# Performance work log

Hardware: AMD Instinct MI355X
Metric: run time of the kernel (lower is better)

The kernel has to match this reference:

```python
import jax, jax.numpy as jnp
import numpy as np

N = 100000   # nodes (in_ch)
D = 128      # emb_ch
E = 1600000  # nonzeros in A_hat
RATE = 0.1   # dropout rate


def setup_inputs() -> dict:
    key = jax.random.key(0)
    k1, k2, k3, k4, k5, k6 = jax.random.split(key, 6)
    x = jnp.arange(N, dtype=jnp.int64) if jax.config.jax_enable_x64 else jnp.arange(N, dtype=jnp.int32)
    rows = jax.random.randint(k1, (E,), 0, N)
    cols = jax.random.randint(k2, (E,), 0, N)
    A_vals = jax.random.uniform(k3, (E,), dtype=jnp.float32)
    # xavier_uniform for [N, D]: bound = sqrt(6/(N+D))
    bound = float(np.sqrt(6.0 / (N + D)))
    emb_weight = jax.random.uniform(k4, (N, D), jnp.float32, -bound, bound)
    u1 = jax.random.uniform(k5, (N, D), dtype=jnp.float32)
    u2 = jax.random.uniform(k6, (N, D), dtype=jnp.float32)
    return {"x": x, "rows": rows, "cols": cols, "A_vals": A_vals,
            "emb_weight": emb_weight, "u1": u1, "u2": u2}


def _dropout(h, u):
    keep = (u >= RATE).astype(h.dtype)
    return h * keep / (1.0 - RATE)


def _spmm(rows, cols, vals, h):
    # out[i] = sum_{e: rows[e]==i} vals[e] * h[cols[e]]  -- COO SpMM
    msgs = vals[:, None] * h[cols]  # [E, D]
    return jax.ops.segment_sum(msgs, rows, num_segments=N)


def reference(x, rows, cols, A_vals, emb_weight, u1, u2):
    h0 = emb_weight[x]                       # embedding lookup [N, D]
    h1 = _spmm(rows, cols, A_vals, _dropout(h0, u1))
    h2 = _spmm(rows, cols, A_vals, _dropout(h1, u2))
    return (h0 + h1 + h2) / 3.0
```

## Files before the change

### kernel.cpp

```cpp
#include <hip/hip_runtime.h>
#include <hip/hip_fp16.h>

#define DD 128
#define SCAN_CHUNK 1024
#define G_ROWS 32
#define G_STAGE 1024

typedef float          f32x4 __attribute__((ext_vector_type(4)));
typedef unsigned int   u32x4 __attribute__((ext_vector_type(4)));
typedef unsigned int   u32x2 __attribute__((ext_vector_type(2)));
typedef unsigned short u16x8 __attribute__((ext_vector_type(8)));

struct __align__(8) Edge { int c; float v; };

__device__ __forceinline__ unsigned short f2h(float f) {
    return __half_as_ushort(__float2half(f));
}
__device__ __forceinline__ float2 up2(unsigned int u) {
    __half2 h = *reinterpret_cast<const __half2*>(&u);
    return __half22float2(h);
}

template <typename T>
__device__ __forceinline__ T ldnt(const T* p) { return __builtin_nontemporal_load(p); }
template <typename T>
__device__ __forceinline__ void stnt(T* p, T v) { __builtin_nontemporal_store(v, p); }

__global__ __launch_bounds__(256) void k_g1hist(const float* __restrict__ emb,
                                                const float* __restrict__ u1,
                                                ushort* __restrict__ g1,
                                                const int* __restrict__ rows,
                                                unsigned int* __restrict__ cnt16,
                                                ushort* __restrict__ rank,
                                                int total8, int E) {
    int i = blockIdx.x * 256 + threadIdx.x;
    bool doE = i < E;
    bool doS = i < total8;
    int r = 0;
    if (doE) r = ldnt(rows + i);
    f32x4 hA, hB, uA, uB;
    if (doS) {
        const f32x4* e4 = (const f32x4*)emb;
        const f32x4* a4 = (const f32x4*)u1;
        hA = ldnt(e4 + 2 * (size_t)i);
        hB = ldnt(e4 + 2 * (size_t)i + 1);
        uA = ldnt(a4 + 2 * (size_t)i);
        uB = ldnt(a4 + 2 * (size_t)i + 1);
    }
    if (doE) {
        int sh = (r & 1) << 4;
        unsigned int old = atomicAdd(&cnt16[r >> 1], 1u << sh);
        stnt(rank + i, (ushort)((old >> sh) & 0xFFFFu));
    }
    if (doS) {
        const float s = 1.0f / 0.9f;
        u16x8 g;
        g[0] = f2h((uA.x >= 0.1f) ? hA.x * s : 0.0f);
        g[1] = f2h((uA.y >= 0.1f) ? hA.y * s : 0.0f);
        g[2] = f2h((uA.z >= 0.1f) ? hA.z * s : 0.0f);
        g[3] = f2h((uA.w >= 0.1f) ? hA.w * s : 0.0f);
        g[4] = f2h((uB.x >= 0.1f) ? hB.x * s : 0.0f);
        g[5] = f2h((uB.y >= 0.1f) ? hB.y * s : 0.0f);
        g[6] = f2h((uB.z >= 0.1f) ? hB.z * s : 0.0f);
        g[7] = f2h((uB.w >= 0.1f) ? hB.w * s : 0.0f);
        ((u16x8*)g1)[i] = g;
    }
}

__global__ __launch_bounds__(256) void k_scan1(const unsigned int* __restrict__ cnt16,
                                               int* __restrict__ rs,
                                               int* __restrict__ bsum, int n) {
    __shared__ int s[256];
    int tid = threadIdx.x;
    int base = blockIdx.x * SCAN_CHUNK + tid * 4;
    int c0 = 0, c1 = 0, c2 = 0, c3 = 0;
    if (base < n) {
        unsigned int w0 = cnt16[base >> 1];
        c0 = (int)(w0 & 0xFFFFu);
        c1 = (int)(w0 >> 16);
    }
    if (base + 2 < n) {
        unsigned int w1 = cnt16[(base >> 1) + 1];
        c2 = (int)(w1 & 0xFFFFu);
        c3 = (int)(w1 >> 16);
    }
    int tsum = c0 + c1 + c2 + c3;
    s[tid] = tsum;
    __syncthreads();
    for (int off = 1; off < 256; off <<= 1) {
        int t = (tid >= off) ? s[tid - off] : 0;
        __syncthreads();
        s[tid] += t;
        __syncthreads();
    }
    int excl = s[tid] - tsum;
    if (tid == 255) bsum[blockIdx.x] = s[255];
    if (base < n)     rs[base]     = excl;
    if (base + 1 < n) rs[base + 1] = excl + c0;
    if (base + 2 < n) rs[base + 2] = excl + c0 + c1;
    if (base + 3 < n) rs[base + 3] = excl + c0 + c1 + c2;
}

__global__ __launch_bounds__(256) void k_scan23(int* __restrict__ rs,
                                                const int* __restrict__ bsum,
                                                int nb, int n) {
    __shared__ int s[1024];
    int tid = threadIdx.x;
    for (int i = tid; i < nb; i += 256) s[i] = bsum[i];
    __syncthreads();
    if (tid == 0) {
        int run = 0;
        for (int i = 0; i < nb; ++i) { int t = s[i]; s[i] = run; run += t; }
    }
    __syncthreads();
    int i = blockIdx.x * 256 + tid;
    if (i < n) rs[i] += s[i >> 10];
}

__global__ __launch_bounds__(256) void k_scatter_prep(const int* __restrict__ rows,
                                                      const int* __restrict__ cols,
                                                      const float* __restrict__ vals,
                                                      const int* __restrict__ rs,
                                                      const ushort* __restrict__ rank,
                                                      Edge* __restrict__ ev,
                                                      const float* __restrict__ emb,
                                                      const float* __restrict__ u2,
                                                      ushort* __restrict__ emb16,
                                                      unsigned char* __restrict__ mask2,
                                                      int E, int total8) {
    int i = blockIdx.x * 256 + threadIdx.x;
    bool doE = i < E;
    bool doS = i < total8;
    int r = 0, c = 0; float vv = 0.f; unsigned int rk = 0;
    if (doE) {
        r = ldnt(rows + i);
        c = ldnt(cols + i);
        vv = ldnt(vals + i);
        rk = ldnt(rank + i);
    }
    f32x4 hA, hB, vA, vB;
    if (doS) {
        const f32x4* e4 = (const f32x4*)emb;
        const f32x4* b4 = (const f32x4*)u2;
        hA = ldnt(e4 + 2 * (size_t)i);
        hB = ldnt(e4 + 2 * (size_t)i + 1);
        vA = ldnt(b4 + 2 * (size_t)i);
        vB = ldnt(b4 + 2 * (size_t)i + 1);
    }
    if (doE) {
        int pos = rs[r] + (int)rk;
        u32x2 q;
        q.x = (unsigned int)c;
        q.y = __float_as_uint(vv);
        ((u32x2*)ev)[pos] = q;
    }
    if (doS) {
        u16x8 e16;
        e16[0] = f2h(hA.x); e16[1] = f2h(hA.y); e16[2] = f2h(hA.z); e16[3] = f2h(hA.w);
        e16[4] = f2h(hB.x); e16[5] = f2h(hB.y); e16[6] = f2h(hB.z); e16[7] = f2h(hB.w);
        stnt((u16x8*)emb16 + i, e16);
        unsigned char m =
            (unsigned char)((vA.x >= 0.1f ? 1u : 0u)  | (vA.y >= 0.1f ? 2u : 0u)  |
                            (vA.z >= 0.1f ? 4u : 0u)  | (vA.w >= 0.1f ? 8u : 0u)  |
                            (vB.x >= 0.1f ? 16u : 0u) | (vB.y >= 0.1f ? 32u : 0u) |
                            (vB.z >= 0.1f ? 64u : 0u) | (vB.w >= 0.1f ? 128u : 0u));
        stnt(mask2 + i, m);
    }
}

template <int MODE>
__global__ __launch_bounds__(256) void k_gather(const int* __restrict__ rowstart,
                                                const Edge* __restrict__ ev,
                                                const ushort* __restrict__ srch,
                                                const unsigned char* __restrict__ mask2,
                                                const ushort* __restrict__ emb16,
                                                const ushort* __restrict__ p16in,
                                                ushort* __restrict__ p16out,
                                                ushort* __restrict__ g2,
                                                float* __restrict__ out,
                                                int N, int E) {
    __shared__ int s_rs[G_ROWS + 1];
    __shared__ Edge s_ev[G_STAGE];

    int tid = threadIdx.x;
    int r0 = blockIdx.x * G_ROWS;
    int h = blockIdx.y;
    if (tid <= G_ROWS) {
        int r = r0 + tid;
        s_rs[tid] = (r < N) ? rowstart[r] : E;
    }
    __syncthreads();
    int base = s_rs[0];
    int nblk = s_rs[G_ROWS] - base;
    int nstage = nblk < G_STAGE ? nblk : G_STAGE;
    for (int i = tid; i < nstage; i += 256) {
        u32x2 q = ldnt((const u32x2*)(ev + base + i));
        Edge ed; ed.c = (int)q.x; ed.v = __uint_as_float(q.y);
        s_ev[i] = ed;
    }
    __syncthreads();

    int grp = tid >> 3;
    int lane = tid & 7;
    int row = r0 + grp;
    if (row >= N) return;
    int start = s_rs[grp] - base;
    int end = s_rs[grp + 1] - base;
    int eL = end < nstage ? end : nstage;

    const u32x4* __restrict__ s4 = (const u32x4*)srch;
    const Edge* __restrict__ evg = ev + base;
    int hoff = (h << 3) + lane;
    float a0 = 0.f, a1 = 0.f, a2 = 0.f, a3 = 0.f;
    float a4 = 0.f, a5 = 0.f, a6 = 0.f, a7 = 0.f;

#define LDE(i) Edge E##i = s_ev[e + i]; float fv##i = E##i.v;
#define LDP(i) int ix##i = e + i; bool ok##i = ix##i < eL; \
               Edge E##i = s_ev[ok##i ? ix##i : last]; \
               float fv##i = ok##i ? E##i.v : 0.0f;
#define GQ(i)  u32x4 q##i = s4[((size_t)E##i.c << 4) + hoff];
#define ACC(i) { float vv = fv##i; \
        float2 w0 = up2(q##i.x), w1 = up2(q##i.y), w2 = up2(q##i.z), w3 = up2(q##i.w); \
        a0 = fmaf(vv, w0.x, a0); a1 = fmaf(vv, w0.y, a1); \
        a2 = fmaf(vv, w1.x, a2); a3 = fmaf(vv, w1.y, a3); \
        a4 = fmaf(vv, w2.x, a4); a5 = fmaf(vv, w2.y, a5); \
        a6 = fmaf(vv, w3.x, a6); a7 = fmaf(vv, w3.y, a7); }

    int e = start;
    for (; e + 8 <= eL; e += 8) {
        LDE(0) LDE(1) LDE(2) LDE(3) LDE(4) LDE(5) LDE(6) LDE(7)
        GQ(0) GQ(1) GQ(2) GQ(3) GQ(4) GQ(5) GQ(6) GQ(7)
        ACC(0) ACC(1) ACC(2) ACC(3) ACC(4) ACC(5) ACC(6) ACC(7)
    }
    if (e < eL) {
        int last = eL - 1;
        LDP(0) LDP(1) LDP(2) LDP(3) LDP(4) LDP(5) LDP(6) LDP(7)
        GQ(0) GQ(1) GQ(2) GQ(3) GQ(4) GQ(5) GQ(6) GQ(7)
        ACC(0) ACC(1) ACC(2) ACC(3) ACC(4) ACC(5) ACC(6) ACC(7)
        e = eL;
    }
    for (; e < end; ++e) {
        Edge E0; { u32x2 q_ = ldnt((const u32x2*)(evg + e));
                   E0.c = (int)q_.x; E0.v = __uint_as_float(q_.y); }
        float fv0 = E0.v;
        GQ(0) ACC(0)
    }
#undef LDE
#undef LDP
#undef GQ
#undef ACC

    size_t o = ((size_t)row << 7) + ((size_t)h << 6) + (size_t)lane * 8;
    if (MODE == 1) {
        unsigned int m = mask2[(size_t)row * 16 + (h << 3) + lane];
        const float s = 1.0f / 0.9f;
        u16x8 gg;
        gg[0] = (m & 1u)   ? f2h(a0 * s) : (ushort)0;
        gg[1] = (m & 2u)   ? f2h(a1 * s) : (ushort)0;
        gg[2] = (m & 4u)   ? f2h(a2 * s) : (ushort)0;
        gg[3] = (m & 8u)   ? f2h(a3 * s) : (ushort)0;
        gg[4] = (m & 16u)  ? f2h(a4 * s) : (ushort)0;
        gg[5] = (m & 32u)  ? f2h(a5 * s) : (ushort)0;
        gg[6] = (m & 64u)  ? f2h(a6 * s) : (ushort)0;
        gg[7] = (m & 128u) ? f2h(a7 * s) : (ushort)0;
        stnt((u16x8*)(g2 + o), gg);
        u16x8 pp;
        pp[0] = f2h(a0); pp[1] = f2h(a1); pp[2] = f2h(a2); pp[3] = f2h(a3);
        pp[4] = f2h(a4); pp[5] = f2h(a5); pp[6] = f2h(a6); pp[7] = f2h(a7);
        stnt((u16x8*)(p16out + o), pp);
    } else {
        u32x4 eq = ldnt((const u32x4*)(emb16 + o));
        u32x4 pq = ldnt((const u32x4*)(p16in + o));
        float2 e0 = up2(eq.x), e1 = up2(eq.y), e2 = up2(eq.z), e3 = up2(eq.w);
        float2 p0 = up2(pq.x), p1 = up2(pq.y), p2 = up2(pq.z), p3 = up2(pq.w);
        const float t3 = 1.0f / 3.0f;
        f32x4 rA, rB;
        rA.x = (e0.x + p0.x + a0) * t3;
        rA.y = (e0.y + p0.y + a1) * t3;
        rA.z = (e1.x + p1.x + a2) * t3;
        rA.w = (e1.y + p1.y + a3) * t3;
        rB.x = (e2.x + p2.x + a4) * t3;
        rB.y = (e2.y + p2.y + a5) * t3;
        rB.z = (e3.x + p3.x + a6) * t3;
        rB.w = (e3.y + p3.y + a7) * t3;
        stnt((f32x4*)(out + o), rA);
        stnt((f32x4*)(out + o) + 1, rB);
    }
}


extern "C" void kernel_launch(void* const* d_in, const int* in_sizes, int n_in,
                              void* d_out, int out_size, void* d_ws, size_t ws_size,
                              hipStream_t stream) {
    const int* rows = (const int*)d_in[1];
    const int* cols = (const int*)d_in[2];
    const float* vals = (const float*)d_in[3];
    const float* emb = (const float*)d_in[4];
    const float* u1 = (const float*)d_in[5];
    const float* u2 = (const float*)d_in[6];
    float* out = (float*)d_out;

    const int N = in_sizes[0];
    const int E = in_sizes[1];
    const size_t ND = (size_t)N * DD;
    const int NW = (N + 1) / 2;

    char* ws = (char*)d_ws;
    Edge* ev     = (Edge*)ws;   ws += (size_t)E * sizeof(Edge);
    ushort* g1   = (ushort*)ws; ws += ND * sizeof(ushort);
    ushort* g2   = (ushort*)ws; ws += ND * sizeof(ushort);
    ushort* p16  = (ushort*)ws; ws += ND * sizeof(ushort);
    ushort* emb16= (ushort*)ws; ws += ND * sizeof(ushort);
    unsigned int* cnt16 = (unsigned int*)ws; ws += (size_t)NW * 4;
    int* rs      = (int*)ws;    ws += (size_t)N * sizeof(int);
    ushort* rank = (ushort*)ws; ws += (size_t)E * sizeof(ushort);
    int* bsum    = (int*)ws;    ws += 4096;
    unsigned char* mask2 = (unsigned char*)ws;

    const int total8 = (int)(ND / 8);
    const int prepBlocks = (total8 + 255) / 256;
    const int gridE = (E + 255) / 256;
    const int gridFuse = prepBlocks > gridE ? prepBlocks : gridE;
    const int nScanBlocks = (N + SCAN_CHUNK - 1) / SCAN_CHUNK;
    const int gridRowX = (N + G_ROWS - 1) / G_ROWS;
    dim3 gridRow(gridRowX, 2, 1);

    hipMemsetAsync(cnt16, 0, (size_t)NW * 4, stream);
    k_g1hist<<<gridFuse, 256, 0, stream>>>(emb, u1, g1, rows, cnt16, rank,
                                           total8, E);
    k_scan1<<<nScanBlocks, 256, 0, stream>>>(cnt16, rs, bsum, N);
    k_scan23<<<(N + 255) / 256, 256, 0, stream>>>(rs, bsum, nScanBlocks, N);
    k_scatter_prep<<<gridFuse, 256, 0, stream>>>(rows, cols, vals, rs, rank,
                                                 ev, emb, u2, emb16, mask2,
                                                 E, total8);
    k_gather<1><<<gridRow, 256, 0, stream>>>(rs, ev, g1, mask2, nullptr, nullptr,
                                             p16, g2, nullptr, N, E);
    k_gather<2><<<gridRow, 256, 0, stream>>>(rs, ev, g2, nullptr, emb16, p16,
                                             nullptr, nullptr, out, N, E);
}
```

Before: 404.2 us.

## Merge all stages into one cooperative persistent kernel with grid syncs

Replaces the memset and six separate kernel launches with one cooperative kernel that runs each stage in grid-stride loops, separated by grid-wide barriers. The fp16 embedding copy and the second dropout mask are now built in the first pass, which leaves the scatter pass touching only edge data. The goal is to remove launch gaps and per-kernel tail effects. The cost is grid.sync overhead, occupancy limited by the launch-bounds hint, and persistent tiles looping serially through the gather phases. A multi-kernel fallback is kept.

```diff
diff --git a/kernel.cpp b/kernel.cpp
--- a/kernel.cpp
+++ b/kernel.cpp
@@ -1,5 +1,8 @@
 #include <hip/hip_runtime.h>
 #include <hip/hip_fp16.h>
+#include <hip/hip_cooperative_groups.h>
+
+namespace cg = cooperative_groups;
 
 #define DD 128
 #define SCAN_CHUNK 1024
@@ -13,6 +16,15 @@
 
 struct __align__(8) Edge { int c; float v; };
 
+struct KArgs {
+    const int* rows; const int* cols; const float* vals;
+    const float* emb; const float* u1; const float* u2;
+    ushort* g1; ushort* g2; ushort* p16; ushort* emb16;
+    unsigned int* cnt16; int* rs; ushort* rank; int* bsum;
+    unsigned char* mask2; Edge* ev; float* out;
+    int N, E, total8, dom1, nScanBlocks, nTilesX, NW;
+};
+
 __device__ __forceinline__ unsigned short f2h(float f) {
     return __half_as_ushort(__float2half(f));
 }
@@ -26,31 +38,27 @@
 template <typename T>
 __device__ __forceinline__ void stnt(T* p, T v) { __builtin_nontemporal_store(v, p); }
 
-__global__ __launch_bounds__(256) void k_g1hist(const float* __restrict__ emb,
-                                                const float* __restrict__ u1,
-                                                ushort* __restrict__ g1,
-                                                const int* __restrict__ rows,
-                                                unsigned int* __restrict__ cnt16,
-                                                ushort* __restrict__ rank,
-                                                int total8, int E) {
-    int i = blockIdx.x * 256 + threadIdx.x;
-    bool doE = i < E;
-    bool doS = i < total8;
+__device__ __forceinline__ void p1_body(const KArgs& a, int i) {
+    bool doE = i < a.E;
+    bool doS = i < a.total8;
     int r = 0;
-    if (doE) r = ldnt(rows + i);
-    f32x4 hA, hB, uA, uB;
+    if (doE) r = ldnt(a.rows + i);
+    f32x4 hA, hB, uA, uB, wA, wB;
     if (doS) {
-        const f32x4* e4 = (const f32x4*)emb;
-        const f32x4* a4 = (const f32x4*)u1;
+        const f32x4* e4 = (const f32x4*)a.emb;
+        const f32x4* a4 = (const f32x4*)a.u1;
+        const f32x4* b4 = (const f32x4*)a.u2;
         hA = ldnt(e4 + 2 * (size_t)i);
         hB = ldnt(e4 + 2 * (size_t)i + 1);
         uA = ldnt(a4 + 2 * (size_t)i);
         uB = ldnt(a4 + 2 * (size_t)i + 1);
+        wA = ldnt(b4 + 2 * (size_t)i);
+        wB = ldnt(b4 + 2 * (size_t)i + 1);
     }
     if (doE) {
         int sh = (r & 1) << 4;
-        unsigned int old = atomicAdd(&cnt16[r >> 1], 1u << sh);
-        stnt(rank + i, (ushort)((old >> sh) & 0xFFFFu));
+        unsigned int old = atomicAdd(&a.cnt16[r >> 1], 1u << sh);
+        stnt(a.rank + i, (ushort)((old >> sh) & 0xFFFFu));
     }
     if (doS) {
         const float s = 1.0f / 0.9f;
@@ -63,26 +71,32 @@
         g[5] = f2h((uB.y >= 0.1f) ? hB.y * s : 0.0f);
         g[6] = f2h((uB.z >= 0.1f) ? hB.z * s : 0.0f);
         g[7] = f2h((uB.w >= 0.1f) ? hB.w * s : 0.0f);
-        ((u16x8*)g1)[i] = g;
-    }
-}
-
-__global__ __launch_bounds__(256) void k_scan1(const unsigned int* __restrict__ cnt16,
-                                               int* __restrict__ rs,
-                                               int* __restrict__ bsum, int n) {
-    __shared__ int s[256];
+        ((u16x8*)a.g1)[i] = g;
+        u16x8 e16;
+        e16[0] = f2h(hA.x); e16[1] = f2h(hA.y); e16[2] = f2h(hA.z); e16[3] = f2h(hA.w);
+        e16[4] = f2h(hB.x); e16[5] = f2h(hB.y); e16[6] = f2h(hB.z); e16[7] = f2h(hB.w);
+        stnt((u16x8*)a.emb16 + i, e16);
+        unsigned char m =
+            (unsigned char)((wA.x >= 0.1f ? 1u : 0u)  | (wA.y >= 0.1f ? 2u : 0u)  |
+                            (wA.z >= 0.1f ? 4u : 0u)  | (wA.w >= 0.1f ? 8u : 0u)  |
+                            (wB.x >= 0.1f ? 16u : 0u) | (wB.y >= 0.1f ? 32u : 0u) |
+                            (wB.z >= 0.1f ? 64u : 0u) | (wB.w >= 0.1f ? 128u : 0u));
+        stnt(a.mask2 + i, m);
+    }
+}
+
+__device__ __forceinline__ void d_scan_chunk(int b, const KArgs& a, int* s) {
     int tid = threadIdx.x;
-    int base = blockIdx.x * SCAN_CHUNK + tid * 4;
+    int n = a.N;
+    int base = b * SCAN_CHUNK + tid * 4;
     int c0 = 0, c1 = 0, c2 = 0, c3 = 0;
     if (base < n) {
-        unsigned int w0 = cnt16[base >> 1];
-        c0 = (int)(w0 & 0xFFFFu);
-        c1 = (int)(w0 >> 16);
+        unsigned int w0 = a.cnt16[base >> 1];
+        c0 = (int)(w0 & 0xFFFFu); c1 = (int)(w0 >> 16);
     }
     if (base + 2 < n) {
-        unsigned int w1 = cnt16[(base >> 1) + 1];
-        c2 = (int)(w1 & 0xFFFFu);
-        c3 = (int)(w1 >> 16);
+        unsigned int w1 = a.cnt16[(base >> 1) + 1];
+        c2 = (int)(w1 & 0xFFFFu); c3 = (int)(w1 >> 16);
     }
     int tsum = c0 + c1 + c2 + c3;
     s[tid] = tsum;
@@ -94,107 +108,41 @@
         __syncthreads();
     }
     int excl = s[tid] - tsum;
-    if (tid == 255) bsum[blockIdx.x] = s[255];
-    if (base < n)     rs[base]     = excl;
-    if (base + 1 < n) rs[base + 1] = excl + c0;
-    if (base + 2 < n) rs[base + 2] = excl + c0 + c1;
-    if (base + 3 < n) rs[base + 3] = excl + c0 + c1 + c2;
-}
-
-__global__ __launch_bounds__(256) void k_scan23(int* __restrict__ rs,
-                                                const int* __restrict__ bsum,
-                                                int nb, int n) {
-    __shared__ int s[1024];
+    if (tid == 255) a.bsum[b] = s[255];
+    if (base < n)     a.rs[base]     = excl;
+    if (base + 1 < n) a.rs[base + 1] = excl + c0;
+    if (base + 2 < n) a.rs[base + 2] = excl + c0 + c1;
+    if (base + 3 < n) a.rs[base + 3] = excl + c0 + c1 + c2;
+}
+
+__device__ __forceinline__ void p3_body(const KArgs& a, int i) {
+    int r = ldnt(a.rows + i);
+    int c = ldnt(a.cols + i);
+    float v = ldnt(a.vals + i);
+    unsigned int rk = ldnt(a.rank + i);
+    int pos = a.rs[r] + (int)rk;
+    u32x2 q;
+    q.x = (unsigned int)c;
+    q.y = __float_as_uint(v);
+    ((u32x2*)a.ev)[pos] = q;
+}
+
+template <int MODE>
+__device__ __forceinline__ void gather_tile(const KArgs& a, int tileX, int h,
+                                            int* s_rs, Edge* s_ev) {
     int tid = threadIdx.x;
-    for (int i = tid; i < nb; i += 256) s[i] = bsum[i];
-    __syncthreads();
-    if (tid == 0) {
-        int run = 0;
-        for (int i = 0; i < nb; ++i) { int t = s[i]; s[i] = run; run += t; }
-    }
-    __syncthreads();
-    int i = blockIdx.x * 256 + tid;
-    if (i < n) rs[i] += s[i >> 10];
-}
-
-__global__ __launch_bounds__(256) void k_scatter_prep(const int* __restrict__ rows,
-                                                      const int* __restrict__ cols,
-                                                      const float* __restrict__ vals,
-                                                      const int* __restrict__ rs,
-                                                      const ushort* __restrict__ rank,
-                                                      Edge* __restrict__ ev,
-                                                      const float* __restrict__ emb,
-                                                      const float* __restrict__ u2,
-                                                      ushort* __restrict__ emb16,
-                                                      unsigned char* __restrict__ mask2,
-                                                      int E, int total8) {
-    int i = blockIdx.x * 256 + threadIdx.x;
-    bool doE = i < E;
-    bool doS = i < total8;
-    int r = 0, c = 0; float vv = 0.f; unsigned int rk = 0;
-    if (doE) {
-        r = ldnt(rows + i);
-        c = ldnt(cols + i);
-        vv = ldnt(vals + i);
-        rk = ldnt(rank + i);
-    }
-    f32x4 hA, hB, vA, vB;
-    if (doS) {
-        const f32x4* e4 = (const f32x4*)emb;
-        const f32x4* b4 = (const f32x4*)u2;
-        hA = ldnt(e4 + 2 * (size_t)i);
-        hB = ldnt(e4 + 2 * (size_t)i + 1);
-        vA = ldnt(b4 + 2 * (size_t)i);
-        vB = ldnt(b4 + 2 * (size_t)i + 1);
-    }
-    if (doE) {
-        int pos = rs[r] + (int)rk;
-        u32x2 q;
-        q.x = (unsigned int)c;
-        q.y = __float_as_uint(vv);
-        ((u32x2*)ev)[pos] = q;
-    }
-    if (doS) {
-        u16x8 e16;
-        e16[0] = f2h(hA.x); e16[1] = f2h(hA.y); e16[2] = f2h(hA.z); e16[3] = f2h(hA.w);
-        e16[4] = f2h(hB.x); e16[5] = f2h(hB.y); e16[6] = f2h(hB.z); e16[7] = f2h(hB.w);
-        stnt((u16x8*)emb16 + i, e16);
-        unsigned char m =
-            (unsigned char)((vA.x >= 0.1f ? 1u : 0u)  | (vA.y >= 0.1f ? 2u : 0u)  |
-                            (vA.z >= 0.1f ? 4u : 0u)  | (vA.w >= 0.1f ? 8u : 0u)  |
-                            (vB.x >= 0.1f ? 16u : 0u) | (vB.y >= 0.1f ? 32u : 0u) |
-                            (vB.z >= 0.1f ? 64u : 0u) | (vB.w >= 0.1f ? 128u : 0u));
-        stnt(mask2 + i, m);
-    }
-}
-
-template <int MODE>
-__global__ __launch_bounds__(256) void k_gather(const int* __restrict__ rowstart,
-                                                const Edge* __restrict__ ev,
-                                                const ushort* __restrict__ srch,
-                                                const unsigned char* __restrict__ mask2,
-                                                const ushort* __restrict__ emb16,
-                                                const ushort* __restrict__ p16in,
-                                                ushort* __restrict__ p16out,
-                                                ushort* __restrict__ g2,
-                                                float* __restrict__ out,
-                                                int N, int E) {
-    __shared__ int s_rs[G_ROWS + 1];
-    __shared__ Edge s_ev[G_STAGE];
-
-    int tid = threadIdx.x;
-    int r0 = blockIdx.x * G_ROWS;
-    int h = blockIdx.y;
+    int r0 = tileX * G_ROWS;
+    __syncthreads();
     if (tid <= G_ROWS) {
         int r = r0 + tid;
-        s_rs[tid] = (r < N) ? rowstart[r] : E;
+        s_rs[tid] = (r < a.N) ? a.rs[r] : a.E;
     }
     __syncthreads();
     int base = s_rs[0];
     int nblk = s_rs[G_ROWS] - base;
     int nstage = nblk < G_STAGE ? nblk : G_STAGE;
     for (int i = tid; i < nstage; i += 256) {
-        u32x2 q = ldnt((const u32x2*)(ev + base + i));
+        u32x2 q = ldnt((const u32x2*)(a.ev + base + i));
         Edge ed; ed.c = (int)q.x; ed.v = __uint_as_float(q.y);
         s_ev[i] = ed;
     }
@@ -203,13 +151,14 @@
     int grp = tid >> 3;
     int lane = tid & 7;
     int row = r0 + grp;
-    if (row >= N) return;
+    if (row >= a.N) return;
     int start = s_rs[grp] - base;
     int end = s_rs[grp + 1] - base;
     int eL = end < nstage ? end : nstage;
 
-    const u32x4* __restrict__ s4 = (const u32x4*)srch;
-    const Edge* __restrict__ evg = ev + base;
+    const ushort* srch = (MODE == 1) ? a.g1 : a.g2;
+    const u32x4* s4 = (const u32x4*)srch;
+    const Edge* evg = a.ev + base;
     int hoff = (h << 3) + lane;
     float a0 = 0.f, a1 = 0.f, a2 = 0.f, a3 = 0.f;
     float a4 = 0.f, a5 = 0.f, a6 = 0.f, a7 = 0.f;
@@ -252,7 +201,7 @@
 
     size_t o = ((size_t)row << 7) + ((size_t)h << 6) + (size_t)lane * 8;
     if (MODE == 1) {
-        unsigned int m = mask2[(size_t)row * 16 + (h << 3) + lane];
+        unsigned int m = a.mask2[(size_t)row * 16 + (h << 3) + lane];
         const float s = 1.0f / 0.9f;
         u16x8 gg;
         gg[0] = (m & 1u)   ? f2h(a0 * s) : (ushort)0;
@@ -263,14 +212,14 @@
         gg[5] = (m & 32u)  ? f2h(a5 * s) : (ushort)0;
         gg[6] = (m & 64u)  ? f2h(a6 * s) : (ushort)0;
         gg[7] = (m & 128u) ? f2h(a7 * s) : (ushort)0;
-        stnt((u16x8*)(g2 + o), gg);
+        stnt((u16x8*)(a.g2 + o), gg);
         u16x8 pp;
         pp[0] = f2h(a0); pp[1] = f2h(a1); pp[2] = f2h(a2); pp[3] = f2h(a3);
         pp[4] = f2h(a4); pp[5] = f2h(a5); pp[6] = f2h(a6); pp[7] = f2h(a7);
-        stnt((u16x8*)(p16out + o), pp);
+        stnt((u16x8*)(a.p16 + o), pp);
     } else {
-        u32x4 eq = ldnt((const u32x4*)(emb16 + o));
-        u32x4 pq = ldnt((const u32x4*)(p16in + o));
+        u32x4 eq = ldnt((const u32x4*)(a.emb16 + o));
+        u32x4 pq = ldnt((const u32x4*)(a.p16 + o));
         float2 e0 = up2(eq.x), e1 = up2(eq.y), e2 = up2(eq.z), e3 = up2(eq.w);
         float2 p0 = up2(pq.x), p1 = up2(pq.y), p2 = up2(pq.z), p3 = up2(pq.w);
         const float t3 = 1.0f / 3.0f;
@@ -283,9 +232,91 @@
         rB.y = (e2.y + p2.y + a5) * t3;
         rB.z = (e3.x + p3.x + a6) * t3;
         rB.w = (e3.y + p3.y + a7) * t3;
-        stnt((f32x4*)(out + o), rA);
-        stnt((f32x4*)(out + o) + 1, rB);
-    }
+        stnt((f32x4*)(a.out + o), rA);
+        stnt((f32x4*)(a.out + o) + 1, rB);
+    }
+}
+
+__global__ __launch_bounds__(256, 6) void k_mega(KArgs a) {
+    cg::grid_group grid = cg::this_grid();
+    __shared__ int s_rs[G_ROWS + 1];
+    __shared__ Edge s_ev[G_STAGE];
+    __shared__ int s_scan[256];
+    __shared__ int s_pref[1024];
+
+    const int NT = (int)gridDim.x * 256;
+    const int tid = threadIdx.x;
+    const int gid = (int)blockIdx.x * 256 + tid;
+
+    for (int i = gid; i < a.NW; i += NT) a.cnt16[i] = 0u;
+    grid.sync();
+
+    for (int i = gid; i < a.dom1; i += NT) p1_body(a, i);
+    grid.sync();
+
+    if ((int)blockIdx.x < a.nScanBlocks) d_scan_chunk((int)blockIdx.x, a, s_scan);
+    grid.sync();
+
+    for (int i = tid; i < a.nScanBlocks; i += 256) s_pref[i] = a.bsum[i];
+    __syncthreads();
+    if (tid == 0) {
+        int run = 0;
+        for (int i = 0; i < a.nScanBlocks; ++i) { int t = s_pref[i]; s_pref[i] = run; run += t; }
+    }
+    __syncthreads();
+    for (int i = gid; i < a.N; i += NT) a.rs[i] += s_pref[i >> 10];
+    grid.sync();
+
+    for (int i = gid; i < a.E; i += NT) p3_body(a, i);
+    grid.sync();
+
+    int nT2 = a.nTilesX * 2;
+    for (int t = (int)blockIdx.x; t < nT2; t += (int)gridDim.x) {
+        int h = (t >= a.nTilesX) ? 1 : 0;
+        int tx = h ? (t - a.nTilesX) : t;
+        gather_tile<1>(a, tx, h, s_rs, s_ev);
+    }
+    grid.sync();
+
+    for (int t = (int)blockIdx.x; t < nT2; t += (int)gridDim.x) {
+        int h = (t >= a.nTilesX) ? 1 : 0;
+        int tx = h ? (t - a.nTilesX) : t;
+        gather_tile<2>(a, tx, h, s_rs, s_ev);
+    }
+}
+
+__global__ __launch_bounds__(256) void k_f_p1(KArgs a) {
+    int gid = blockIdx.x * 256 + threadIdx.x;
+    int NT = gridDim.x * 256;
+    for (int i = gid; i < a.dom1; i += NT) p1_body(a, i);
+}
+__global__ __launch_bounds__(256) void k_f_scan1(KArgs a) {
+    __shared__ int s[256];
+    d_scan_chunk((int)blockIdx.x, a, s);
+}
+__global__ __launch_bounds__(256) void k_f_p2b(KArgs a) {
+    __shared__ int s_pref[1024];
+    int tid = threadIdx.x;
+    for (int i = tid; i < a.nScanBlocks; i += 256) s_pref[i] = a.bsum[i];
+    __syncthreads();
+    if (tid == 0) {
+        int run = 0;
+        for (int i = 0; i < a.nScanBlocks; ++i) { int t = s_pref[i]; s_pref[i] = run; run += t; }
+    }
+    __syncthreads();
+    int i = blockIdx.x * 256 + tid;
+    if (i < a.N) a.rs[i] += s_pref[i >> 10];
+}
+__global__ __launch_bounds__(256) void k_f_p3(KArgs a) {
+    int gid = blockIdx.x * 256 + threadIdx.x;
+    int NT = gridDim.x * 256;
+    for (int i = gid; i < a.E; i += NT) p3_body(a, i);
+}
+template <int MODE>
+__global__ __launch_bounds__(256) void k_f_g(KArgs a) {
+    __shared__ int s_rs[G_ROWS + 1];
+    __shared__ Edge s_ev[G_STAGE];
+    gather_tile<MODE>(a, (int)blockIdx.x, (int)blockIdx.y, s_rs, s_ev);
 }
 
 
@@ -318,23 +349,54 @@
     unsigned char* mask2 = (unsigned char*)ws;
 
     const int total8 = (int)(ND / 8);
-    const int prepBlocks = (total8 + 255) / 256;
-    const int gridE = (E + 255) / 256;
-    const int gridFuse = prepBlocks > gridE ? prepBlocks : gridE;
+    const int dom1 = total8 > E ? total8 : E;
     const int nScanBlocks = (N + SCAN_CHUNK - 1) / SCAN_CHUNK;
-    const int gridRowX = (N + G_ROWS - 1) / G_ROWS;
-    dim3 gridRow(gridRowX, 2, 1);
-
-    hipMemsetAsync(cnt16, 0, (size_t)NW * 4, stream);
-    k_g1hist<<<gridFuse, 256, 0, stream>>>(emb, u1, g1, rows, cnt16, rank,
-                                           total8, E);
-    k_scan1<<<nScanBlocks, 256, 0, stream>>>(cnt16, rs, bsum, N);
-    k_scan23<<<(N + 255) / 256, 256, 0, stream>>>(rs, bsum, nScanBlocks, N);
-    k_scatter_prep<<<gridFuse, 256, 0, stream>>>(rows, cols, vals, rs, rank,
-                                                 ev, emb, u2, emb16, mask2,
-                                                 E, total8);
-    k_gather<1><<<gridRow, 256, 0, stream>>>(rs, ev, g1, mask2, nullptr, nullptr,
-                                             p16, g2, nullptr, N, E);
-    k_gather<2><<<gridRow, 256, 0, stream>>>(rs, ev, g2, nullptr, emb16, p16,
-                                             nullptr, nullptr, out, N, E);
-}
+    const int nTilesX = (N + G_ROWS - 1) / G_ROWS;
+
+    KArgs ka;
+    ka.rows = rows; ka.cols = cols; ka.vals = vals;
+    ka.emb = emb; ka.u1 = u1; ka.u2 = u2;
+    ka.g1 = g1; ka.g2 = g2; ka.p16 = p16; ka.emb16 = emb16;
+    ka.cnt16 = cnt16; ka.rs = rs; ka.rank = rank; ka.bsum = bsum;
+    ka.mask2 = mask2; ka.ev = ev; ka.out = out;
+    ka.N = N; ka.E = E; ka.total8 = total8; ka.dom1 = dom1;
+    ka.nScanBlocks = nScanBlocks; ka.nTilesX = nTilesX; ka.NW = NW;
+
+    static int NB = 0;
+    static bool coopOK = true;
+    if (NB == 0) {
+        int dev = 0;
+        hipGetDevice(&dev);
+        hipDeviceProp_t prop{};
+        hipGetDeviceProperties(&prop, dev);
+        int nbcu = 0;
+        hipError_t oe = hipOccupancyMaxActiveBlocksPerMultiprocessor(&nbcu, k_mega, 256, 0);
+        if (oe != hipSuccess || nbcu < 1 || !prop.cooperativeLaunch) coopOK = false;
+        int ncu = prop.multiProcessorCount > 0 ? prop.multiProcessorCount : 256;
+        NB = (nbcu < 1 ? 1 : nbcu) * ncu;
+        if (NB < 256) NB = 256;
+        if (NB > 8192) NB = 8192;
+    }
+
+    bool launched = false;
+    if (coopOK) {
+        void* params[] = { (void*)&ka };
+        hipError_t err = hipLaunchCooperativeKernel((const void*)k_mega, dim3(NB),
+                                                    dim3(256), params, 0, stream);
+        if (err == hipSuccess) {
+            launched = true;
+        } else {
+            coopOK = false;
+            (void)hipGetLastError();
+        }
+    }
+    if (!launched) {
+        hipMemsetAsync(cnt16, 0, (size_t)NW * 4, stream);
+        k_f_p1<<<(dom1 + 255) / 256, 256, 0, stream>>>(ka);
+        k_f_scan1<<<nScanBlocks, 256, 0, stream>>>(ka);
+        k_f_p2b<<<(N + 255) / 256, 256, 0, stream>>>(ka);
+        k_f_p3<<<(E + 255) / 256, 256, 0, stream>>>(ka);
+        k_f_g<1><<<dim3(nTilesX, 2), 256, 0, stream>>>(ka);
+        k_f_g<2><<<dim3(nTilesX, 2), 256, 0, stream>>>(ka);
+    }
+}
```

Measured after the change: 955.8 us. 136% more time.
